# Performance work log

Hardware: AMD Instinct MI355X
Metric: run time of the kernel (lower is better)

The kernel has to match this reference:

```python
import jax, jax.numpy as jnp
import numpy as np

B, S, D, H, L, K = 16, 384, 512, 8, 4, 7
HD = D // H
MAXLEN = 400


def _pos_encoding(d=D, max_len=MAXLEN):
    # Faithful to the (unusual) torch loop: even idx i -> sin(pos/10000**(2i/d)),
    # odd idx i+1 -> cos(pos/10000**(2(i+1)/d))
    pe = np.zeros((max_len, d), dtype=np.float32)
    pos = np.arange(max_len, dtype=np.float64)[:, None]
    i = np.arange(0, d, 2)
    pe[:, i] = np.sin(pos / 10000.0 ** (2 * i / d))
    pe[:, i + 1] = np.cos(pos / 10000.0 ** (2 * (i + 1) / d))
    return jnp.asarray(pe)

POS_ENC = _pos_encoding()


def layer_norm(x, g, b, eps=1e-5):
    m = jnp.mean(x, -1, keepdims=True)
    v = jnp.mean((x - m) ** 2, -1, keepdims=True)
    return (x - m) * jax.lax.rsqrt(v + eps) * g + b


def dsconv(x, dw_w, pw_w, pw_b):
    # x: [B,S,D]; depthwise conv1d (no bias) then pointwise 1x1 (bias)
    xc = jnp.transpose(x, (0, 2, 1))  # [B,D,S]
    y = jax.lax.conv_general_dilated(
        xc, dw_w, window_strides=(1,), padding=[(K // 2, K // 2)],
        dimension_numbers=("NCH", "OIH", "NCH"), feature_group_count=D)  # [B,D,S]
    return jnp.einsum("bcs,oc->bso", y, pw_w) + pw_b  # [B,S,D]


def setup_inputs():
    key = jax.random.key(0)
    ks = jax.random.split(key, 16)
    sc = 0.02
    inp = {
        "x": jax.random.normal(ks[0], (B, S, D), jnp.float32),
        "mask": jax.random.randint(ks[1], (B, S), 0, 2, jnp.int32),
        "dw_w": jax.random.normal(ks[2], (L, D, 1, K), jnp.float32) * sc,
        "pw_w": jax.random.normal(ks[3], (L, D, D), jnp.float32) * sc,
        "pw_b": jnp.zeros((L, D), jnp.float32),
        "conv_ln_g": jnp.ones((L, D), jnp.float32),
        "conv_ln_b": jnp.zeros((L, D), jnp.float32),
        "pos_ln_g": jnp.ones((D,), jnp.float32),
        "pos_ln_b": jnp.zeros((D,), jnp.float32),
        "wq": jax.random.normal(ks[4], (D, D), jnp.float32) * sc,
        "bq": jnp.zeros((D,), jnp.float32),
        "wk": jax.random.normal(ks[5], (D, D), jnp.float32) * sc,
        "bk": jnp.zeros((D,), jnp.float32),
        "wv": jax.random.normal(ks[6], (D, D), jnp.float32) * sc,
        "bv": jnp.zeros((D,), jnp.float32),
        "wo": jax.random.normal(ks[7], (D, D), jnp.float32) * sc,
        "bo": jnp.zeros((D,), jnp.float32),
        "ff_ln_g": jnp.ones((D,), jnp.float32),
        "ff_ln_b": jnp.zeros((D,), jnp.float32),
        "ff_w": jax.random.normal(ks[8], (D, D), jnp.float32) * sc,
        "ff_b": jnp.zeros((D,), jnp.float32),
    }
    return inp


def attention(x, mask, wq, bq, wk, bk, wv, bv, wo, bo):
    def heads(w, b):
        y = jnp.einsum("bsd,od->bso", x, w) + b
        return jnp.transpose(y.reshape(B, S, H, HD), (0, 2, 1, 3))  # [B,H,S,HD]
    q, k, v = heads(wq, bq), heads(wk, bk), heads(wv, bv)
    energy = jnp.einsum("bhqd,bhkd->bhqk", q, k) / jnp.sqrt(jnp.float32(HD))
    m = (mask == 1)[:, None, None, :]  # [B,1,1,S]
    energy = jnp.where(m, jnp.float32(-1e10), energy)
    alpha = jax.nn.softmax(energy, axis=-1)  # dropout = identity (eval)
    a = jnp.einsum("bhqk,bhkd->bhqd", alpha, v)
    a = jnp.transpose(a, (0, 2, 1, 3)).reshape(B, S, D)
    return jnp.einsum("bsd,od->bso", a, wo) + bo


def reference(x, mask, dw_w, pw_w, pw_b, conv_ln_g, conv_ln_b, pos_ln_g, pos_ln_b,
              wq, bq, wk, bk, wv, bv, wo, bo, ff_ln_g, ff_ln_b, ff_w, ff_b):
    out = x + POS_ENC[None, :S, :]
    res = out
    out = layer_norm(out, pos_ln_g, pos_ln_b)
    for i in range(L):
        out = jax.nn.relu(dsconv(out, dw_w[i], pw_w[i], pw_b[i]))
        out = out + res  # dropout = identity (eval)
        res = out
        out = layer_norm(out, conv_ln_g[i], conv_ln_b[i])
    out = attention(out, mask, wq, bq, wk, bk, wv, bv, wo, bo)
    out = out + res
    res = out
    out = layer_norm(out, ff_ln_g, ff_ln_b)
    out = jax.nn.relu(jnp.einsum("bsd,od->bso", out, ff_w) + ff_b)
    return out + res
```

## Files before the change

### kernel.cpp

```cpp
#include <hip/hip_runtime.h>

#define BB 16
#define SS 384
#define DD 512
#define HH 8
#define HDIM 64
#define LLAY 4
#define KW 7
#define MM (BB*SS)

typedef unsigned short u16;
typedef unsigned int u32;
typedef short short8v __attribute__((ext_vector_type(8)));
typedef float floatx4 __attribute__((ext_vector_type(4)));

__device__ __forceinline__ float bf2f(u16 u) {
    union { u32 i; float f; } v; v.i = ((u32)u) << 16; return v.f;
}
__device__ __forceinline__ u16 f2bf(float f) {
    union { float f; u32 i; } v; v.f = f;
    return (u16)((v.i + 0x7FFFu + ((v.i >> 16) & 1u)) >> 16);
}
__device__ __forceinline__ bool sniff_f32(const void* dtp) {
    return *((const u32*)dtp) == 0x3F800000u;
}
__device__ __forceinline__ float ldf(const void* p, long i, bool f32) {
    return f32 ? ((const float*)p)[i] : bf2f(((const u16*)p)[i]);
}
__device__ __forceinline__ short8v ldfrag_scalar(const void* p, long i, bool f32) {
    short8v r;
    if (f32) {
        const float* q = (const float*)p + i;
#pragma unroll
        for (int j = 0; j < 8; j++) r[j] = (short)f2bf(q[j]);
    } else {
        r = *(const short8v*)((const u16*)p + i);
    }
    return r;
}

__device__ __forceinline__ void load_lds16(const u16* g, u16* l) {
    __builtin_amdgcn_global_load_lds((const __attribute__((address_space(1))) void*)g,
                                     (__attribute__((address_space(3))) void*)l, 16, 0, 0);
}
__device__ __forceinline__ int swz(int row) { return (row & 3) ^ ((row >> 2) & 3); }
__device__ __forceinline__ short8v lds_frag(const u16* buf, int row, int quad) {
    return *(const short8v*)(buf + ((size_t)row * 4 + (quad ^ swz(row))) * 8);
}

#define WCV_DW 2359296
#define WCV_TOT (WCV_DW + LLAY*KW*DD)
__global__ __launch_bounds__(256) void cvt_weights_kernel(
    const void* __restrict__ pw_w, const void* __restrict__ wq,
    const void* __restrict__ wk, const void* __restrict__ wv,
    const void* __restrict__ wo, const void* __restrict__ ff_w,
    const void* __restrict__ dw_w,
    u16* __restrict__ dst, const void* __restrict__ dtp) {
    const bool f32 = sniff_f32(dtp);
    const int i = blockIdx.x * 256 + threadIdx.x;
    if (i >= WCV_TOT) return;
    const void* src; long idx;
    if (i < 1048576) { src = pw_w; idx = i; }
    else if (i < WCV_DW) {
        const int j = i - 1048576;
        const int m = j >> 18;
        idx = j & 262143;
        src = (m == 0) ? wq : (m == 1) ? wk : (m == 2) ? wv : (m == 3) ? wo : ff_w;
    } else {
        const int j = i - WCV_DW;
        const int l = j / (KW * DD);
        const int r1 = j % (KW * DD);
        const int t = r1 / DD, c = r1 % DD;
        src = dw_w; idx = ((long)l * DD + c) * KW + t;
    }
    dst[i] = f2bf(ldf(src, idx, f32));
}

__global__ __launch_bounds__(256) void posln_kernel(const void* __restrict__ x,
                                                    const void* __restrict__ g,
                                                    const void* __restrict__ bvec,
                                                    u16* __restrict__ res,
                                                    u16* __restrict__ out,
                                                    const void* __restrict__ dtp) {
    const bool f32 = sniff_f32(dtp);
    const int row = blockIdx.x;
    const int s = row % SS;
    const int tid = threadIdx.x;
    float v[2];
#pragma unroll
    for (int i = 0; i < 2; i++) {
        const int d = tid + i * 256;
        const float freq = __expf(-(float)d * 0.035977892078032f);
        const float arg = (float)s * freq;
        const float pe = (d & 1) ? cosf(arg) : sinf(arg);
        v[i] = ldf(x, (long)row * DD + d, f32) + pe;
        res[row * DD + d] = f2bf(v[i]);
    }
    float sum = v[0] + v[1], sq = v[0] * v[0] + v[1] * v[1];
#pragma unroll
    for (int off = 32; off; off >>= 1) { sum += __shfl_down(sum, off); sq += __shfl_down(sq, off); }
    __shared__ float red[4][2];
    const int wv = tid >> 6;
    if ((tid & 63) == 0) { red[wv][0] = sum; red[wv][1] = sq; }
    __syncthreads();
    sum = red[0][0] + red[1][0] + red[2][0] + red[3][0];
    sq  = red[0][1] + red[1][1] + red[2][1] + red[3][1];
    const float mean = sum * (1.f / DD);
    const float rstd = rsqrtf(sq * (1.f / DD) - mean * mean + 1e-5f);
#pragma unroll
    for (int i = 0; i < 2; i++) {
        const int d = tid + i * 256;
        out[row * DD + d] = f2bf((v[i] - mean) * rstd * ldf(g, d, f32) + ldf(bvec, d, f32));
    }
}

template <int VEC>
__global__ __launch_bounds__(256) void dwconv_kernel(const u16* __restrict__ in,
                                                     const void* __restrict__ w, int layer,
                                                     u16* __restrict__ out,
                                                     const void* __restrict__ dtp) {
    if constexpr (VEC) {
        const int bsw = (blockIdx.x & 7) * (MM * DD / 8 / 256 / 8) + (blockIdx.x >> 3);
        const int idx = bsw * 256 + threadIdx.x;
        const int c8 = (idx & 63) * 8;
        const int ms = idx >> 6;
        const int s = ms % SS;
        const u16* wl = (const u16*)w + (size_t)layer * KW * DD;
        float acc[8] = {0, 0, 0, 0, 0, 0, 0, 0};
#pragma unroll
        for (int t = 0; t < KW; t++) {
            const int ss2 = s + t - 3;
            if (ss2 >= 0 && ss2 < SS) {
                const short8v iv = *(const short8v*)(in + (size_t)(ms + t - 3) * DD + c8);
                const short8v wv = *(const short8v*)(wl + t * DD + c8);
#pragma unroll
                for (int j = 0; j < 8; j++)
                    acc[j] += bf2f((u16)iv[j]) * bf2f((u16)wv[j]);
            }
        }
        short8v ov;
#pragma unroll
        for (int j = 0; j < 8; j++) ov[j] = (short)f2bf(acc[j]);
        *(short8v*)(out + (size_t)ms * DD + c8) = ov;
    } else {
        const bool f32 = sniff_f32(dtp);
        const long woff = (long)layer * DD * KW;
        const int idx = blockIdx.x * 256 + threadIdx.x;
        const int c = idx & (DD - 1);
        const int ms = idx >> 9;
        const int s = ms % SS;
        float acc = 0.f;
#pragma unroll
        for (int t = 0; t < KW; t++) {
            const int ss2 = s + t - 3;
            if (ss2 >= 0 && ss2 < SS)
                acc += bf2f(in[(ms + t - 3) * DD + c]) * ldf(w, woff + c * KW + t, f32);
        }
        out[idx] = f2bf(acc);
    }
}

__device__ __forceinline__ void stage_tile(const u16* A, const u16* W, int m0,
                                           u16* Abuf, u16* Wbuf, int tid, int k0) {
#pragma unroll
    for (int j = 0; j < 8; j++) {
        const int c = j * 256 + tid;
        const int row = c >> 2;
        const int kpart = (c & 3) ^ swz(row);
        load_lds16(W + (size_t)row * DD + k0 + kpart * 8, Wbuf + (size_t)c * 8);
    }
    if (tid < 128) {
        const int row = tid >> 2;
        const int kpart = (tid & 3) ^ swz(row);
        load_lds16(A + (size_t)(m0 + row) * DD + k0 + kpart * 8, Abuf + (size_t)tid * 8);
    }
}

__device__ __forceinline__ void kloop_lds(const u16* A, const u16* W, int m0,
                                          u16* Abuf, u16* Wbuf,
                                          int tid, int wave, int ln15, int quad,
                                          floatx4 acc[2][8]) {
    stage_tile(A, W, m0, Abuf, Wbuf, tid, 0);
    __syncthreads();
    for (int ks = 0; ks < 16; ks++) {
        const int cur = ks & 1;
        u16* Ab = Abuf + cur * (32 * 32);
        u16* Wb = Wbuf + cur * (DD * 32);
        if (ks < 15)
            stage_tile(A, W, m0, Abuf + (cur ^ 1) * (32 * 32),
                       Wbuf + (cur ^ 1) * (DD * 32), tid, (ks + 1) * 32);
        const short8v a0 = lds_frag(Ab, ln15, quad);
        const short8v a1 = lds_frag(Ab, 16 + ln15, quad);
#pragma unroll
        for (int nt = 0; nt < 8; nt++) {
            const short8v b = lds_frag(Wb, wave * 128 + nt * 16 + ln15, quad);
            acc[0][nt] = __builtin_amdgcn_mfma_f32_16x16x32_bf16(a0, b, acc[0][nt], 0, 0, 0);
            acc[1][nt] = __builtin_amdgcn_mfma_f32_16x16x32_bf16(a1, b, acc[1][nt], 0, 0, 0);
        }
        __syncthreads();
    }
}

template <int RELU, int DO_LN, int FINAL, int WVEC>
__global__ __launch_bounds__(256, 2) void gemm32_kernel(
    const u16* __restrict__ A, const void* __restrict__ W, int wlayer,
    const void* __restrict__ bias, const void* __restrict__ g,
    const void* __restrict__ bvec, int blayer,
    const u16* __restrict__ res_in, u16* __restrict__ res_out,
    void* __restrict__ out, const void* __restrict__ dtp) {
    const bool f32 = sniff_f32(dtp);
    const long woff = (long)wlayer * DD * DD;
    const long voff = (long)blayer * DD;
    __shared__ float part[4][2][16][2];
    __shared__ __align__(16) u16 Wbuf[2 * DD * 32];
    __shared__ __align__(16) u16 Abuf[2 * 32 * 32];
    const int tid = threadIdx.x;
    const int m0 = blockIdx.x * 32;
    const int wave = tid >> 6, lane = tid & 63;
    const int ln15 = lane & 15, quad = lane >> 4;

    floatx4 acc[2][8];
#pragma unroll
    for (int mt = 0; mt < 2; mt++)
#pragma unroll
        for (int nt = 0; nt < 8; nt++) acc[mt][nt] = {0.f, 0.f, 0.f, 0.f};

    if constexpr (WVEC) {
        kloop_lds(A, (const u16*)W + woff, m0, Abuf, Wbuf, tid, wave, ln15, quad, acc);
    } else {
        const u16* A0 = A + (size_t)(m0 + ln15) * DD + quad * 8;
        const u16* A1 = A0 + 16 * DD;
#pragma unroll
        for (int ks = 0; ks < 16; ks++) {
            const int k0 = ks * 32;
            short8v a0 = *(const short8v*)(A0 + k0);
            short8v a1 = *(const short8v*)(A1 + k0);
            short8v b[8];
#pragma unroll
            for (int nt = 0; nt < 8; nt++) {
                const long wrow = woff + (long)(wave * 128 + nt * 16 + ln15) * DD + quad * 8 + k0;
                b[nt] = ldfrag_scalar(W, wrow, f32);
            }
#pragma unroll
            for (int nt = 0; nt < 8; nt++) {
                acc[0][nt] = __builtin_amdgcn_mfma_f32_16x16x32_bf16(a0, b[nt], acc[0][nt], 0, 0, 0);
                acc[1][nt] = __builtin_amdgcn_mfma_f32_16x16x32_bf16(a1, b[nt], acc[1][nt], 0, 0, 0);
            }
        }
    }

#pragma unroll
    for (int nt = 0; nt < 8; nt++) {
        const int col = wave * 128 + nt * 16 + ln15;
        const float bval = ldf(bias, voff + col, f32);
#pragma unroll
        for (int mt = 0; mt < 2; mt++)
#pragma unroll
            for (int r = 0; r < 4; r++) {
                const int m = m0 + mt * 16 + quad * 4 + r;
                float y = acc[mt][nt][r] + bval;
                if (RELU) y = fmaxf(y, 0.f);
                y += bf2f(res_in[(size_t)m * DD + col]);
                if (res_out) res_out[(size_t)m * DD + col] = f2bf(y);
                acc[mt][nt][r] = y;
            }
    }
    if constexpr (DO_LN) {
        float ls[2][4], lq[2][4];
#pragma unroll
        for (int mt = 0; mt < 2; mt++)
#pragma unroll
            for (int r = 0; r < 4; r++) {
                float s = 0.f, q = 0.f;
#pragma unroll
                for (int nt = 0; nt < 8; nt++) { const float y = acc[mt][nt][r]; s += y; q += y * y; }
                ls[mt][r] = s; lq[mt][r] = q;
            }
#pragma unroll
        for (int off = 1; off < 16; off <<= 1)
#pragma unroll
            for (int mt = 0; mt < 2; mt++)
#pragma unroll
                for (int r = 0; r < 4; r++) {
                    ls[mt][r] += __shfl_xor(ls[mt][r], off);
                    lq[mt][r] += __shfl_xor(lq[mt][r], off);
                }
        if (ln15 == 0) {
#pragma unroll
            for (int mt = 0; mt < 2; mt++)
#pragma unroll
                for (int r = 0; r < 4; r++) {
                    part[wave][mt][quad * 4 + r][0] = ls[mt][r];
                    part[wave][mt][quad * 4 + r][1] = lq[mt][r];
                }
        }
        __syncthreads();
        float mean[2][4], rstd[2][4];
#pragma unroll
        for (int mt = 0; mt < 2; mt++)
#pragma unroll
            for (int r = 0; r < 4; r++) {
                const int rr = quad * 4 + r;
                const float s = part[0][mt][rr][0] + part[1][mt][rr][0] + part[2][mt][rr][0] + part[3][mt][rr][0];
                const float q = part[0][mt][rr][1] + part[1][mt][rr][1] + part[2][mt][rr][1] + part[3][mt][rr][1];
                const float mn = s * (1.f / DD);
                mean[mt][r] = mn;
                rstd[mt][r] = rsqrtf(q * (1.f / DD) - mn * mn + 1e-5f);
            }
#pragma unroll
        for (int nt = 0; nt < 8; nt++) {
            const int col = wave * 128 + nt * 16 + ln15;
            const float gv = ldf(g, voff + col, f32);
            const float bv = ldf(bvec, voff + col, f32);
#pragma unroll
            for (int mt = 0; mt < 2; mt++)
#pragma unroll
                for (int r = 0; r < 4; r++) {
                    const int m = m0 + mt * 16 + quad * 4 + r;
                    ((u16*)out)[(size_t)m * DD + col] =
                        f2bf((acc[mt][nt][r] - mean[mt][r]) * rstd[mt][r] * gv + bv);
                }
        }
    } else {
#pragma unroll
        for (int nt = 0; nt < 8; nt++) {
            const int col = wave * 128 + nt * 16 + ln15;
#pragma unroll
            for (int mt = 0; mt < 2; mt++)
#pragma unroll
                for (int r = 0; r < 4; r++) {
                    const int m = m0 + mt * 16 + quad * 4 + r;
                    if (FINAL && f32) ((float*)out)[(size_t)m * DD + col] = acc[mt][nt][r];
                    else              ((u16*)out)[(size_t)m * DD + col] = f2bf(acc[mt][nt][r]);
                }
        }
    }
}

#define VPAD 40
template <int WVEC>
__global__ __launch_bounds__(256, 2) void qkv32_kernel(
    const u16* __restrict__ A,
    const void* __restrict__ Wq, const void* __restrict__ Wk, const void* __restrict__ Wv,
    const void* __restrict__ bq, const void* __restrict__ bk, const void* __restrict__ bv,
    u16* __restrict__ qo, u16* __restrict__ ko, u16* __restrict__ vo,
    const void* __restrict__ dtp) {
    const bool f32 = sniff_f32(dtp);
    const int sel = blockIdx.y;
    const void* W = (sel == 0) ? Wq : (sel == 1) ? Wk : Wv;
    const void* bias = (sel == 0) ? bq : (sel == 1) ? bk : bv;
    u16* out = (sel == 0) ? qo : (sel == 1) ? ko : vo;

    __shared__ __align__(16) u16 Wbuf[2 * DD * 32];
    __shared__ __align__(16) u16 Abuf[2 * 32 * 32];
    u16 (*vtile)[128][VPAD] = (u16 (*)[128][VPAD])Wbuf;

    const int tid = threadIdx.x;
    const int m0 = blockIdx.x * 32;
    const int wave = tid >> 6, lane = tid & 63;
    const int ln15 = lane & 15, quad = lane >> 4;
    const int bidx = m0 / SS;

    floatx4 acc[2][8];
#pragma unroll
    for (int mt = 0; mt < 2; mt++)
#pragma unroll
        for (int nt = 0; nt < 8; nt++) acc[mt][nt] = {0.f, 0.f, 0.f, 0.f};

    if constexpr (WVEC) {
        kloop_lds(A, (const u16*)W, m0, Abuf, Wbuf, tid, wave, ln15, quad, acc);
    } else {
        const u16* A0 = A + (size_t)(m0 + ln15) * DD + quad * 8;
        const u16* A1 = A0 + 16 * DD;
#pragma unroll
        for (int ks = 0; ks < 16; ks++) {
            const int k0 = ks * 32;
            short8v a0 = *(const short8v*)(A0 + k0);
            short8v a1 = *(const short8v*)(A1 + k0);
            short8v b[8];
#pragma unroll
            for (int nt = 0; nt < 8; nt++) {
                const long wrow = (long)(wave * 128 + nt * 16 + ln15) * DD + quad * 8 + k0;
                b[nt] = ldfrag_scalar(W, wrow, f32);
            }
#pragma unroll
            for (int nt = 0; nt < 8; nt++) {
                acc[0][nt] = __builtin_amdgcn_mfma_f32_16x16x32_bf16(a0, b[nt], acc[0][nt], 0, 0, 0);
                acc[1][nt] = __builtin_amdgcn_mfma_f32_16x16x32_bf16(a1, b[nt], acc[1][nt], 0, 0, 0);
            }
        }
    }

    if (sel == 2) {
#pragma unroll
        for (int nt = 0; nt < 8; nt++) {
            const int c = nt * 16 + ln15;
            const float bval = ldf(bias, wave * 128 + c, f32);
#pragma unroll
            for (int mt = 0; mt < 2; mt++)
#pragma unroll
                for (int r = 0; r < 4; r++)
                    vtile[wave][c][mt * 16 + quad * 4 + r] = f2bf(acc[mt][nt][r] + bval);
        }
        __builtin_amdgcn_s_waitcnt(0);
#pragma unroll
        for (int cc = 0; cc < 2; cc++) {
            const int c = lane * 2 + cc;
            const int col = wave * 128 + c;
            const int h = col >> 6, hd = col & 63;
            u16* dst = vo + ((size_t)(bidx * HH + h) * HDIM + hd) * SS + (m0 - bidx * SS);
            const u16* srcl = &vtile[wave][c][0];
#pragma unroll
            for (int j = 0; j < 4; j++)
                *(short8v*)(dst + j * 8) = *(const short8v*)(srcl + j * 8);
        }
    } else {
#pragma unroll
        for (int nt = 0; nt < 8; nt++) {
            const int col = wave * 128 + nt * 16 + ln15;
            const int h = col >> 6, hd = col & 63;
            const float bval = ldf(bias, col, f32);
#pragma unroll
            for (int mt = 0; mt < 2; mt++)
#pragma unroll
                for (int r = 0; r < 4; r++) {
                    const int m = m0 + mt * 16 + quad * 4 + r;
                    const int s = m - bidx * SS;
                    out[((size_t)(bidx * HH + h) * SS + s) * HDIM + hd] = f2bf(acc[mt][nt][r] + bval);
                }
        }
    }
}

#define SSPF 388
#define SSPH 392
__global__ __launch_bounds__(256) void attn_kernel(const u16* __restrict__ q,
                                                   const u16* __restrict__ k,
                                                   const u16* __restrict__ vT,
                                                   const int* __restrict__ mask,
                                                   u16* __restrict__ out) {
    __shared__ float sc[16 * SSPF];
    __shared__ float rsum[16];
    u16* al = (u16*)sc;

    const int n = blockIdx.x;
    const int i = n >> 3;
    const int g = (n & 7) * 16 + i / 24;
    const int qt = i % 24;
    const int h = g & 7, b = g >> 3;
    const int q0 = qt * 16;
    const int wave = threadIdx.x >> 6, lane = threadIdx.x & 63;
    const int ln15 = lane & 15, quad = lane >> 4;

    const u16* qh = q + (size_t)(b * HH + h) * SS * HDIM;
    const u16* kh = k + (size_t)(b * HH + h) * SS * HDIM;

    const short8v* arow = (const short8v*)(qh + (q0 + ln15) * HDIM + quad * 8);
    const short8v a0 = arow[0], a1 = arow[4];
#pragma unroll
    for (int t = 0; t < 6; t++) {
        const int n0 = wave * 96 + t * 16;
        const short8v* brow = (const short8v*)(kh + (n0 + ln15) * HDIM + quad * 8);
        floatx4 acc = {0.f, 0.f, 0.f, 0.f};
        __builtin_amdgcn_s_setprio(1);
        acc = __builtin_amdgcn_mfma_f32_16x16x32_bf16(a0, brow[0], acc, 0, 0, 0);
        acc = __builtin_amdgcn_mfma_f32_16x16x32_bf16(a1, brow[4], acc, 0, 0, 0);
        __builtin_amdgcn_s_setprio(0);
        const int kk = n0 + ln15;
        const bool msk = (mask[b * SS + kk] == 1);
#pragma unroll
        for (int r = 0; r < 4; r++) {
            float v = acc[r] * 0.125f;
            if (msk) v = -1e10f;
            sc[(quad * 4 + r) * SSPF + kk] = v;
        }
    }
    __syncthreads();
    const int r = threadIdx.x >> 4, cg = threadIdx.x & 15;
    float pv[24], mx = -3.0e38f;
#pragma unroll
    for (int j = 0; j < 24; j++) { pv[j] = sc[r * SSPF + cg + 16 * j]; mx = fmaxf(mx, pv[j]); }
#pragma unroll
    for (int off = 8; off; off >>= 1) mx = fmaxf(mx, __shfl_xor(mx, off, 16));
    float sum = 0.f;
#pragma unroll
    for (int j = 0; j < 24; j++) { const float p = __expf(pv[j] - mx); pv[j] = p; sum += p; }
#pragma unroll
    for (int off = 8; off; off >>= 1) sum += __shfl_xor(sum, off, 16);
    if (cg == 0) rsum[r] = sum;
    __syncthreads();
#pragma unroll
    for (int j = 0; j < 24; j++) al[r * SSPH + cg + 16 * j] = f2bf(pv[j]);
    __syncthreads();
    const u16* vh = vT + (size_t)(b * HH + h) * HDIM * SS;
    const int d0 = wave * 16;
    floatx4 acc = {0.f, 0.f, 0.f, 0.f};
    __builtin_amdgcn_s_setprio(1);
#pragma unroll
    for (int k0 = 0; k0 < SS; k0 += 32) {
        const short8v af = *(const short8v*)(al + ln15 * SSPH + k0 + quad * 8);
        const short8v bf = *(const short8v*)(vh + (d0 + ln15) * SS + k0 + quad * 8);
        acc = __builtin_amdgcn_mfma_f32_16x16x32_bf16(af, bf, acc, 0, 0, 0);
    }
    __builtin_amdgcn_s_setprio(0);
#pragma unroll
    for (int rr = 0; rr < 4; rr++) {
        const int lr = quad * 4 + rr;
        const int s = q0 + lr;
        out[((size_t)(b * SS + s)) * DD + h * HDIM + d0 + ln15] = f2bf(acc[rr] / rsum[lr]);
    }
}

extern "C" void kernel_launch(void* const* d_in, const int* in_sizes, int n_in,
                              void* d_out, int out_size, void* d_ws, size_t ws_size,
                              hipStream_t stream) {
    (void)in_sizes; (void)n_in; (void)out_size;
    const void* x     = d_in[0];
    const int*  mask  = (const int*)d_in[1];
    const void* dw_w  = d_in[2];
    const void* pw_w  = d_in[3];
    const void* pw_b  = d_in[4];
    const void* cln_g = d_in[5];
    const void* cln_b = d_in[6];
    const void* pln_g = d_in[7];
    const void* pln_b = d_in[8];
    const void* wq    = d_in[9];
    const void* bq    = d_in[10];
    const void* wk    = d_in[11];
    const void* bk    = d_in[12];
    const void* wv    = d_in[13];
    const void* bv    = d_in[14];
    const void* wo    = d_in[15];
    const void* bo    = d_in[16];
    const void* fln_g = d_in[17];
    const void* fln_b = d_in[18];
    const void* ff_w  = d_in[19];
    const void* ff_b  = d_in[20];
    const void* dtp   = cln_g;

    const size_t nAct = (size_t)MM * DD;
    char* p = (char*)d_ws;
    u16* res   = (u16*)p; p += nAct * 2;
    u16* lnout = (u16*)p; p += nAct * 2;
    u16* tmp   = (u16*)p; p += nAct * 2;
    u16* vT    = (u16*)p; p += nAct * 2;
    u16* wcv   = (u16*)p;
    u16* kb    = (u16*)d_out;

    const size_t needFast = nAct * 2 * 4 + (size_t)WCV_TOT * 2;
    const bool fast = (ws_size >= needFast);

    posln_kernel<<<MM, 256, 0, stream>>>(x, pln_g, pln_b, res, lnout, dtp);

    if (fast) {
        cvt_weights_kernel<<<(WCV_TOT + 255) / 256, 256, 0, stream>>>(
            pw_w, wq, wk, wv, wo, ff_w, dw_w, wcv, dtp);
        const u16* w_pw = wcv;
        const u16* w_q  = wcv + 1048576;
        const u16* w_k  = wcv + 1310720;
        const u16* w_v  = wcv + 1572864;
        const u16* w_o  = wcv + 1835008;
        const u16* w_ff = wcv + 2097152;
        const u16* w_dw = wcv + WCV_DW;

        for (int i = 0; i < LLAY; i++) {
            dwconv_kernel<1><<<MM * DD / 8 / 256, 256, 0, stream>>>(lnout, w_dw, i, tmp, dtp);
            gemm32_kernel<1, 1, 0, 1><<<MM / 32, 256, 0, stream>>>(
                tmp, w_pw + (size_t)i * DD * DD, 0, pw_b, cln_g, cln_b, i,
                res, res, lnout, dtp);
        }
        qkv32_kernel<1><<<dim3(MM / 32, 3), 256, 0, stream>>>(
            lnout, w_q, w_k, w_v, bq, bk, bv, tmp, kb, vT, dtp);

        attn_kernel<<<BB * HH * (SS / 16), 256, 0, stream>>>(tmp, kb, vT, mask, lnout);

        gemm32_kernel<0, 1, 0, 1><<<MM / 32, 256, 0, stream>>>(
            lnout, w_o, 0, bo, fln_g, fln_b, 0, res, res, lnout, dtp);
        gemm32_kernel<1, 0, 1, 1><<<MM / 32, 256, 0, stream>>>(
            lnout, w_ff, 0, ff_b, nullptr, nullptr, 0, res, nullptr, d_out, dtp);
    } else {
        for (int i = 0; i < LLAY; i++) {
            dwconv_kernel<0><<<MM * DD / 256, 256, 0, stream>>>(lnout, dw_w, i, tmp, dtp);
            gemm32_kernel<1, 1, 0, 0><<<MM / 32, 256, 0, stream>>>(
                tmp, pw_w, i, pw_b, cln_g, cln_b, i, res, res, lnout, dtp);
        }
        qkv32_kernel<0><<<dim3(MM / 32, 3), 256, 0, stream>>>(
            lnout, wq, wk, wv, bq, bk, bv, tmp, kb, vT, dtp);

        attn_kernel<<<BB * HH * (SS / 16), 256, 0, stream>>>(tmp, kb, vT, mask, lnout);

        gemm32_kernel<0, 1, 0, 0><<<MM / 32, 256, 0, stream>>>(
            lnout, wo, 0, bo, fln_g, fln_b, 0, res, res, lnout, dtp);
        gemm32_kernel<1, 0, 1, 0><<<MM / 32, 256, 0, stream>>>(
            lnout, ff_w, 0, ff_b, nullptr, nullptr, 0, res, nullptr, d_out, dtp);
    }
}
```

Baseline: 384.4 us.

## Fuse depthwise conv into pointwise GEMM staging and merge posln with weight conversion

The depthwise 7-tap conv is computed inside the pointwise GEMM's k-loop from a 38-row halo tile staged in LDS, so the separate dwconv kernel and its intermediate activation round-trip are gone. Ping-pong buffers alternate between lnout and tmp. The positional-encoding layernorm and the weight conversion are merged into one launch, and fast sin/cos intrinsics are used. In exchange, each GEMM block does redundant conv arithmetic per k-step on VALU, which could stall the MFMA loop. The halo rows at the batch edges rely on per-row masking.

```diff
diff --git a/kernel.cpp b/kernel.cpp
--- a/kernel.cpp
+++ b/kernel.cpp
@@ -50,49 +50,47 @@
 
 #define WCV_DW 2359296
 #define WCV_TOT (WCV_DW + LLAY*KW*DD)
-__global__ __launch_bounds__(256) void cvt_weights_kernel(
+#define NCVB ((WCV_TOT + 255) / 256)
+
+__global__ __launch_bounds__(256) void posln_cvt_kernel(
+    const void* __restrict__ x, const void* __restrict__ g, const void* __restrict__ bvec,
+    u16* __restrict__ res, u16* __restrict__ out,
     const void* __restrict__ pw_w, const void* __restrict__ wq,
     const void* __restrict__ wk, const void* __restrict__ wv,
     const void* __restrict__ wo, const void* __restrict__ ff_w,
-    const void* __restrict__ dw_w,
-    u16* __restrict__ dst, const void* __restrict__ dtp) {
+    const void* __restrict__ dw_w, u16* __restrict__ wdst,
+    const void* __restrict__ dtp) {
     const bool f32 = sniff_f32(dtp);
-    const int i = blockIdx.x * 256 + threadIdx.x;
-    if (i >= WCV_TOT) return;
-    const void* src; long idx;
-    if (i < 1048576) { src = pw_w; idx = i; }
-    else if (i < WCV_DW) {
-        const int j = i - 1048576;
-        const int m = j >> 18;
-        idx = j & 262143;
-        src = (m == 0) ? wq : (m == 1) ? wk : (m == 2) ? wv : (m == 3) ? wo : ff_w;
-    } else {
-        const int j = i - WCV_DW;
-        const int l = j / (KW * DD);
-        const int r1 = j % (KW * DD);
-        const int t = r1 / DD, c = r1 % DD;
-        src = dw_w; idx = ((long)l * DD + c) * KW + t;
-    }
-    dst[i] = f2bf(ldf(src, idx, f32));
-}
-
-__global__ __launch_bounds__(256) void posln_kernel(const void* __restrict__ x,
-                                                    const void* __restrict__ g,
-                                                    const void* __restrict__ bvec,
-                                                    u16* __restrict__ res,
-                                                    u16* __restrict__ out,
-                                                    const void* __restrict__ dtp) {
-    const bool f32 = sniff_f32(dtp);
+    const int tid = threadIdx.x;
+    if (blockIdx.x >= MM) {
+        const int i = (blockIdx.x - MM) * 256 + tid;
+        if (i >= WCV_TOT) return;
+        const void* src; long idx;
+        if (i < 1048576) { src = pw_w; idx = i; }
+        else if (i < WCV_DW) {
+            const int j = i - 1048576;
+            const int m = j >> 18;
+            idx = j & 262143;
+            src = (m == 0) ? wq : (m == 1) ? wk : (m == 2) ? wv : (m == 3) ? wo : ff_w;
+        } else {
+            const int j = i - WCV_DW;
+            const int l = j / (KW * DD);
+            const int r1 = j % (KW * DD);
+            const int t = r1 / DD, c = r1 % DD;
+            src = dw_w; idx = ((long)l * DD + c) * KW + t;
+        }
+        wdst[i] = f2bf(ldf(src, idx, f32));
+        return;
+    }
     const int row = blockIdx.x;
     const int s = row % SS;
-    const int tid = threadIdx.x;
     float v[2];
 #pragma unroll
     for (int i = 0; i < 2; i++) {
         const int d = tid + i * 256;
         const float freq = __expf(-(float)d * 0.035977892078032f);
         const float arg = (float)s * freq;
-        const float pe = (d & 1) ? cosf(arg) : sinf(arg);
+        const float pe = (d & 1) ? __cosf(arg) : __sinf(arg);
         v[i] = ldf(x, (long)row * DD + d, f32) + pe;
         res[row * DD + d] = f2bf(v[i]);
     }
@@ -100,8 +98,8 @@
 #pragma unroll
     for (int off = 32; off; off >>= 1) { sum += __shfl_down(sum, off); sq += __shfl_down(sq, off); }
     __shared__ float red[4][2];
-    const int wv = tid >> 6;
-    if ((tid & 63) == 0) { red[wv][0] = sum; red[wv][1] = sq; }
+    const int wv2 = tid >> 6;
+    if ((tid & 63) == 0) { red[wv2][0] = sum; red[wv2][1] = sq; }
     __syncthreads();
     sum = red[0][0] + red[1][0] + red[2][0] + red[3][0];
     sq  = red[0][1] + red[1][1] + red[2][1] + red[3][1];
@@ -114,50 +112,24 @@
     }
 }
 
-template <int VEC>
 __global__ __launch_bounds__(256) void dwconv_kernel(const u16* __restrict__ in,
                                                      const void* __restrict__ w, int layer,
                                                      u16* __restrict__ out,
                                                      const void* __restrict__ dtp) {
-    if constexpr (VEC) {
-        const int bsw = (blockIdx.x & 7) * (MM * DD / 8 / 256 / 8) + (blockIdx.x >> 3);
-        const int idx = bsw * 256 + threadIdx.x;
-        const int c8 = (idx & 63) * 8;
-        const int ms = idx >> 6;
-        const int s = ms % SS;
-        const u16* wl = (const u16*)w + (size_t)layer * KW * DD;
-        float acc[8] = {0, 0, 0, 0, 0, 0, 0, 0};
-#pragma unroll
-        for (int t = 0; t < KW; t++) {
-            const int ss2 = s + t - 3;
-            if (ss2 >= 0 && ss2 < SS) {
-                const short8v iv = *(const short8v*)(in + (size_t)(ms + t - 3) * DD + c8);
-                const short8v wv = *(const short8v*)(wl + t * DD + c8);
-#pragma unroll
-                for (int j = 0; j < 8; j++)
-                    acc[j] += bf2f((u16)iv[j]) * bf2f((u16)wv[j]);
-            }
-        }
-        short8v ov;
-#pragma unroll
-        for (int j = 0; j < 8; j++) ov[j] = (short)f2bf(acc[j]);
-        *(short8v*)(out + (size_t)ms * DD + c8) = ov;
-    } else {
-        const bool f32 = sniff_f32(dtp);
-        const long woff = (long)layer * DD * KW;
-        const int idx = blockIdx.x * 256 + threadIdx.x;
-        const int c = idx & (DD - 1);
-        const int ms = idx >> 9;
-        const int s = ms % SS;
-        float acc = 0.f;
-#pragma unroll
-        for (int t = 0; t < KW; t++) {
-            const int ss2 = s + t - 3;
-            if (ss2 >= 0 && ss2 < SS)
-                acc += bf2f(in[(ms + t - 3) * DD + c]) * ldf(w, woff + c * KW + t, f32);
-        }
-        out[idx] = f2bf(acc);
-    }
+    const bool f32 = sniff_f32(dtp);
+    const long woff = (long)layer * DD * KW;
+    const int idx = blockIdx.x * 256 + threadIdx.x;
+    const int c = idx & (DD - 1);
+    const int ms = idx >> 9;
+    const int s = ms % SS;
+    float acc = 0.f;
+#pragma unroll
+    for (int t = 0; t < KW; t++) {
+        const int ss2 = s + t - 3;
+        if (ss2 >= 0 && ss2 < SS)
+            acc += bf2f(in[(ms + t - 3) * DD + c]) * ldf(w, woff + c * KW + t, f32);
+    }
+    out[idx] = f2bf(acc);
 }
 
 __device__ __forceinline__ void stage_tile(const u16* A, const u16* W, int m0,
@@ -201,9 +173,74 @@
     }
 }
 
-template <int RELU, int DO_LN, int FINAL, int WVEC>
+__device__ __forceinline__ void stage_tile_dw(const u16* A, const u16* W, int m0,
+                                              u16* Hb, u16* Wb, int tid, int k0) {
+#pragma unroll
+    for (int j = 0; j < 8; j++) {
+        const int c = j * 256 + tid;
+        const int row = c >> 2;
+        const int kpart = (c & 3) ^ swz(row);
+        load_lds16(W + (size_t)row * DD + k0 + kpart * 8, Wb + (size_t)c * 8);
+    }
+    if (tid < 152) {
+        const int row = tid >> 2, col = tid & 3;
+        load_lds16(A + (long)(m0 - 3 + row) * DD + k0 + col * 8, Hb + (size_t)tid * 8);
+    }
+}
+
+__device__ __forceinline__ void kloop_lds_dw(const u16* A, const u16* W, const u16* wdwg,
+                                             int m0, u16* Hbuf , u16* Wbuf,
+                                             u16* Wdw ,
+                                             int tid, int wave, int ln15, int quad,
+                                             floatx4 acc[2][8]) {
+#pragma unroll
+    for (int j = 0; j < 2; j++) {
+        const int c = j * 256 + tid;
+        if (c < 448) load_lds16(wdwg + (size_t)c * 8, Wdw + (size_t)c * 8);
+    }
+    stage_tile_dw(A, W, m0, Hbuf, Wbuf, tid, 0);
+    __syncthreads();
+    const int s0 = m0 % SS;
+    for (int ks = 0; ks < 16; ks++) {
+        const int cur = ks & 1;
+        u16* Hb = Hbuf + cur * (38 * 32);
+        u16* Wb = Wbuf + cur * (DD * 32);
+        const int k0 = ks * 32;
+        if (ks < 15)
+            stage_tile_dw(A, W, m0, Hbuf + (cur ^ 1) * (38 * 32),
+                          Wbuf + (cur ^ 1) * (DD * 32), tid, (ks + 1) * 32);
+        float c0[8] = {0, 0, 0, 0, 0, 0, 0, 0}, c1[8] = {0, 0, 0, 0, 0, 0, 0, 0};
+#pragma unroll
+        for (int t = 0; t < KW; t++) {
+            const short8v h0 = *(const short8v*)(Hb + (size_t)(ln15 + t) * 32 + quad * 8);
+            const short8v h1 = *(const short8v*)(Hb + (size_t)(16 + ln15 + t) * 32 + quad * 8);
+            const short8v wv = *(const short8v*)(Wdw + (size_t)t * DD + k0 + quad * 8);
+            const bool v0 = (unsigned)(s0 + ln15 + t - 3) < SS;
+            const bool v1 = (unsigned)(s0 + 16 + ln15 + t - 3) < SS;
+#pragma unroll
+            for (int j = 0; j < 8; j++) {
+                const float wj = bf2f((u16)wv[j]);
+                if (v0) c0[j] += bf2f((u16)h0[j]) * wj;
+                if (v1) c1[j] += bf2f((u16)h1[j]) * wj;
+            }
+        }
+        short8v a0, a1;
+#pragma unroll
+        for (int j = 0; j < 8; j++) { a0[j] = (short)f2bf(c0[j]); a1[j] = (short)f2bf(c1[j]); }
+#pragma unroll
+        for (int nt = 0; nt < 8; nt++) {
+            const short8v b = lds_frag(Wb, wave * 128 + nt * 16 + ln15, quad);
+            acc[0][nt] = __builtin_amdgcn_mfma_f32_16x16x32_bf16(a0, b, acc[0][nt], 0, 0, 0);
+            acc[1][nt] = __builtin_amdgcn_mfma_f32_16x16x32_bf16(a1, b, acc[1][nt], 0, 0, 0);
+        }
+        __syncthreads();
+    }
+}
+
+template <int RELU, int DO_LN, int FINAL, int WVEC, int DW>
 __global__ __launch_bounds__(256, 2) void gemm32_kernel(
     const u16* __restrict__ A, const void* __restrict__ W, int wlayer,
+    const u16* __restrict__ dww,
     const void* __restrict__ bias, const void* __restrict__ g,
     const void* __restrict__ bvec, int blayer,
     const u16* __restrict__ res_in, u16* __restrict__ res_out,
@@ -213,7 +250,7 @@
     const long voff = (long)blayer * DD;
     __shared__ float part[4][2][16][2];
     __shared__ __align__(16) u16 Wbuf[2 * DD * 32];
-    __shared__ __align__(16) u16 Abuf[2 * 32 * 32];
+    __shared__ __align__(16) u16 xbuf[6016];
     const int tid = threadIdx.x;
     const int m0 = blockIdx.x * 32;
     const int wave = tid >> 6, lane = tid & 63;
@@ -225,8 +262,11 @@
 #pragma unroll
         for (int nt = 0; nt < 8; nt++) acc[mt][nt] = {0.f, 0.f, 0.f, 0.f};
 
-    if constexpr (WVEC) {
-        kloop_lds(A, (const u16*)W + woff, m0, Abuf, Wbuf, tid, wave, ln15, quad, acc);
+    if constexpr (DW) {
+        kloop_lds_dw(A, (const u16*)W + woff, dww, m0, xbuf, Wbuf, xbuf + 2 * 38 * 32,
+                     tid, wave, ln15, quad, acc);
+    } else if constexpr (WVEC) {
+        kloop_lds(A, (const u16*)W + woff, m0, xbuf, Wbuf, tid, wave, ln15, quad, acc);
     } else {
         const u16* A0 = A + (size_t)(m0 + ln15) * DD + quad * 8;
         const u16* A1 = A0 + 16 * DD;
@@ -550,10 +590,9 @@
     const size_t needFast = nAct * 2 * 4 + (size_t)WCV_TOT * 2;
     const bool fast = (ws_size >= needFast);
 
-    posln_kernel<<<MM, 256, 0, stream>>>(x, pln_g, pln_b, res, lnout, dtp);
-
     if (fast) {
-        cvt_weights_kernel<<<(WCV_TOT + 255) / 256, 256, 0, stream>>>(
+        posln_cvt_kernel<<<MM + NCVB, 256, 0, stream>>>(
+            x, pln_g, pln_b, res, lnout,
             pw_w, wq, wk, wv, wo, ff_w, dw_w, wcv, dtp);
         const u16* w_pw = wcv;
         const u16* w_q  = wcv + 1048576;
@@ -564,34 +603,38 @@
         const u16* w_dw = wcv + WCV_DW;
 
         for (int i = 0; i < LLAY; i++) {
-            dwconv_kernel<1><<<MM * DD / 8 / 256, 256, 0, stream>>>(lnout, w_dw, i, tmp, dtp);
-            gemm32_kernel<1, 1, 0, 1><<<MM / 32, 256, 0, stream>>>(
-                tmp, w_pw + (size_t)i * DD * DD, 0, pw_b, cln_g, cln_b, i,
-                res, res, lnout, dtp);
+            const u16* cin = (i & 1) ? tmp : lnout;
+            u16* cout      = (i & 1) ? lnout : tmp;
+            gemm32_kernel<1, 1, 0, 1, 1><<<MM / 32, 256, 0, stream>>>(
+                cin, w_pw + (size_t)i * DD * DD, 0, w_dw + (size_t)i * KW * DD,
+                pw_b, cln_g, cln_b, i, res, res, cout, dtp);
         }
         qkv32_kernel<1><<<dim3(MM / 32, 3), 256, 0, stream>>>(
             lnout, w_q, w_k, w_v, bq, bk, bv, tmp, kb, vT, dtp);
 
         attn_kernel<<<BB * HH * (SS / 16), 256, 0, stream>>>(tmp, kb, vT, mask, lnout);
 
-        gemm32_kernel<0, 1, 0, 1><<<MM / 32, 256, 0, stream>>>(
-            lnout, w_o, 0, bo, fln_g, fln_b, 0, res, res, lnout, dtp);
-        gemm32_kernel<1, 0, 1, 1><<<MM / 32, 256, 0, stream>>>(
-            lnout, w_ff, 0, ff_b, nullptr, nullptr, 0, res, nullptr, d_out, dtp);
+        gemm32_kernel<0, 1, 0, 1, 0><<<MM / 32, 256, 0, stream>>>(
+            lnout, w_o, 0, nullptr, bo, fln_g, fln_b, 0, res, res, lnout, dtp);
+        gemm32_kernel<1, 0, 1, 1, 0><<<MM / 32, 256, 0, stream>>>(
+            lnout, w_ff, 0, nullptr, ff_b, nullptr, nullptr, 0, res, nullptr, d_out, dtp);
     } else {
+        posln_cvt_kernel<<<MM, 256, 0, stream>>>(
+            x, pln_g, pln_b, res, lnout,
+            pw_w, wq, wk, wv, wo, ff_w, dw_w, (u16*)d_ws, dtp);
         for (int i = 0; i < LLAY; i++) {
-            dwconv_kernel<0><<<MM * DD / 256, 256, 0, stream>>>(lnout, dw_w, i, tmp, dtp);
-            gemm32_kernel<1, 1, 0, 0><<<MM / 32, 256, 0, stream>>>(
-                tmp, pw_w, i, pw_b, cln_g, cln_b, i, res, res, lnout, dtp);
+            dwconv_kernel<<<MM * DD / 256, 256, 0, stream>>>(lnout, dw_w, i, tmp, dtp);
+            gemm32_kernel<1, 1, 0, 0, 0><<<MM / 32, 256, 0, stream>>>(
+                tmp, pw_w, i, nullptr, pw_b, cln_g, cln_b, i, res, res, lnout, dtp);
         }
         qkv32_kernel<0><<<dim3(MM / 32, 3), 256, 0, stream>>>(
             lnout, wq, wk, wv, bq, bk, bv, tmp, kb, vT, dtp);
 
         attn_kernel<<<BB * HH * (SS / 16), 256, 0, stream>>>(tmp, kb, vT, mask, lnout);
 
-        gemm32_kernel<0, 1, 0, 0><<<MM / 32, 256, 0, stream>>>(
-            lnout, wo, 0, bo, fln_g, fln_b, 0, res, res, lnout, dtp);
-        gemm32_kernel<1, 0, 1, 0><<<MM / 32, 256, 0, stream>>>(
-            lnout, ff_w, 0, ff_b, nullptr, nullptr, 0, res, nullptr, d_out, dtp);
-    }
-}
+        gemm32_kernel<0, 1, 0, 0, 0><<<MM / 32, 256, 0, stream>>>(
+            lnout, wo, 0, nullptr, bo, fln_g, fln_b, 0, res, res, lnout, dtp);
+        gemm32_kernel<1, 0, 1, 0, 0><<<MM / 32, 256, 0, stream>>>(
+            lnout, ff_w, 0, nullptr, ff_b, nullptr, nullptr, 0, res, nullptr, d_out, dtp);
+    }
+}
```

Result: slower. 399.0 us (+3.8%).
